# Kernel optimization log

Measured on AMD Instinct MI355X. Metric: run time of the kernel, lower is better.

Reference implementation:

```python
import jax, jax.numpy as jnp
import numpy as np

N_NODES = 50000
N_EDGES = 800000
IN_F = 128
OUT_F = 64
NEG_SLOPE = 0.2  # GATConv default leaky relu slope

def setup_inputs() -> dict:
    key = jax.random.key(0)
    k1, k2, k3, k4, k5 = jax.random.split(key, 5)
    x = jax.random.normal(k1, (N_NODES, IN_F), dtype=jnp.float32)
    edge_index = jax.random.randint(k2, (2, N_EDGES), 0, N_NODES, dtype=jnp.int64)
    W = jax.random.normal(k3, (IN_F, OUT_F), dtype=jnp.float32) * (1.0 / np.sqrt(IN_F))
    att_src = jax.random.normal(k4, (OUT_F,), dtype=jnp.float32) * 0.1
    att_dst = jax.random.normal(k5, (OUT_F,), dtype=jnp.float32) * 0.1
    bias = jnp.zeros((OUT_F,), dtype=jnp.float32)
    return {"x": x, "edge_index": edge_index, "W": W, "att_src": att_src, "att_dst": att_dst, "bias": bias}

def reference(x, edge_index, W, att_src, att_dst, bias):
    N = x.shape[0]
    h = x @ W  # [N, out]
    # GATConv adds self-loops by default
    loops = jnp.arange(N, dtype=edge_index.dtype)
    src = jnp.concatenate([edge_index[0], loops])  # message sources (neighbors j)
    dst = jnp.concatenate([edge_index[1], loops])  # targets i (softmax segments)
    a_src = h @ att_src  # [N]
    a_dst = h @ att_dst  # [N]
    e = a_src[src] + a_dst[dst]  # [E+N]
    e = jnp.where(e > 0, e, NEG_SLOPE * e)
    # segment softmax over incoming edges of each target node
    e_max = jax.ops.segment_max(e, dst, num_segments=N)
    p = jnp.exp(e - e_max[dst])
    denom = jax.ops.segment_sum(p, dst, num_segments=N)
    alpha = p / (denom[dst] + 1e-16)  # [E+N]
    # scatter-add aggregate weighted source features
    out = jax.ops.segment_sum(h[src] * alpha[:, None], dst, num_segments=N)  # [N, out]
    out = jax.nn.relu(out + bias)
    return out[None]  # wrapper unsqueezes: [1, N, out]
```

## Files before the change

### kernel.cpp

```cpp
#include <hip/hip_runtime.h>
#include <math.h>

#define N_NODES 50000
#define N_EDGES 800000
#define IN_F 128
#define OUT_F 64
#define NEG_SLOPE 0.2f

#define CAP 64
#define GB 196
#define TPW 4
#define PSZ 128
#define NPART ((N_NODES + PSZ - 1) / PSZ)
#define PADCAP 3072
#define CHUNK 2048
#define NCHUNK ((N_EDGES + CHUNK - 1) / CHUNK)

typedef __attribute__((ext_vector_type(8))) short bf16x8;
typedef __attribute__((ext_vector_type(4))) float f32x4;

__device__ __forceinline__ unsigned short f2bf(float f) {
    unsigned u = __float_as_uint(f);
    return (unsigned short)((u + 0x7FFFu + ((u >> 16) & 1u)) >> 16);
}
__device__ __forceinline__ float bf_lo(unsigned u) { return __uint_as_float(u << 16); }
__device__ __forceinline__ float bf_hi(unsigned u) { return __uint_as_float(u & 0xFFFF0000u); }

__global__ __launch_bounds__(256) void k_fused(
    const float* __restrict__ x, const float* __restrict__ W,
    const float* __restrict__ att_src, const float* __restrict__ att_dst,
    const int* __restrict__ ei, unsigned short* __restrict__ h,
    float* __restrict__ a_src, float* __restrict__ a_dst,
    int* __restrict__ gcnt, unsigned* __restrict__ glist) {
    int tid = threadIdx.x;

    if (blockIdx.x >= GB) {
        __shared__ int bcnt[NPART];
        __shared__ int bbase[NPART];
        int f = blockIdx.x - GB;
        for (int i = tid; i < NPART; i += 256) bcnt[i] = 0;
        __syncthreads();

        int e0 = f * CHUNK + tid * 8;
        bool val = e0 < N_EDGES;
        int sv[8], dv[8], sl[8];
        if (val) {
            const int4 sa = *reinterpret_cast<const int4*>(ei + e0);
            const int4 sb = *reinterpret_cast<const int4*>(ei + e0 + 4);
            const int4 da = *reinterpret_cast<const int4*>(ei + N_EDGES + e0);
            const int4 db = *reinterpret_cast<const int4*>(ei + N_EDGES + e0 + 4);
            sv[0]=sa.x; sv[1]=sa.y; sv[2]=sa.z; sv[3]=sa.w;
            sv[4]=sb.x; sv[5]=sb.y; sv[6]=sb.z; sv[7]=sb.w;
            dv[0]=da.x; dv[1]=da.y; dv[2]=da.z; dv[3]=da.w;
            dv[4]=db.x; dv[5]=db.y; dv[6]=db.z; dv[7]=db.w;
#pragma unroll
            for (int i = 0; i < 8; ++i)
                sl[i] = atomicAdd(&bcnt[dv[i] >> 7], 1);
        }
        __syncthreads();
        for (int i = tid; i < NPART; i += 256)
            bbase[i] = bcnt[i] ? atomicAdd(&gcnt[i], bcnt[i]) : 0;
        __syncthreads();
        if (val) {
#pragma unroll
            for (int i = 0; i < 8; ++i) {
                int p = dv[i] >> 7;
                int idx = bbase[p] + sl[i];
                if (idx < PADCAP)
                    glist[(size_t)p * PADCAP + idx] =
                        (unsigned)(sv[i] & 0xFFFF) | ((unsigned)(dv[i] & (PSZ - 1)) << 16);
            }
        }
        return;
    }

    int w = tid >> 6;
    int lane = tid & 63;
    int col = lane & 15;
    int kg = lane >> 4;
    int gw = blockIdx.x * 4 + w;

    bf16x8 bf[4][4];
#pragma unroll
    for (int ks = 0; ks < 4; ++ks)
#pragma unroll
        for (int nt = 0; nt < 4; ++nt) {
            bf16x8 b;
#pragma unroll
            for (int i = 0; i < 8; ++i)
                b[i] = (short)f2bf(W[(ks * 32 + kg * 8 + i) * OUT_F + col * 4 + nt]);
            bf[ks][nt] = b;
        }
    float asv[4], adv[4];
#pragma unroll
    for (int nt = 0; nt < 4; ++nt) {
        asv[nt] = att_src[col * 4 + nt];
        adv[nt] = att_dst[col * 4 + nt];
    }

    for (int it = 0; it < TPW; ++it) {
        int r0 = (gw * TPW + it) * 16;
        if (r0 >= N_NODES) break;
        int arow = min(r0 + col, N_NODES - 1);
        const float* xp = &x[(size_t)arow * IN_F + kg * 8];

        bf16x8 af[4];
#pragma unroll
        for (int ks = 0; ks < 4; ++ks) {
            float4 xa = *reinterpret_cast<const float4*>(xp + ks * 32);
            float4 xb = *reinterpret_cast<const float4*>(xp + ks * 32 + 4);
            bf16x8 a;
            a[0] = (short)f2bf(xa.x); a[1] = (short)f2bf(xa.y);
            a[2] = (short)f2bf(xa.z); a[3] = (short)f2bf(xa.w);
            a[4] = (short)f2bf(xb.x); a[5] = (short)f2bf(xb.y);
            a[6] = (short)f2bf(xb.z); a[7] = (short)f2bf(xb.w);
            af[ks] = a;
        }

        f32x4 acc[4];
        f32x4 z = {0.f, 0.f, 0.f, 0.f};
#pragma unroll
        for (int nt = 0; nt < 4; ++nt) acc[nt] = z;
#pragma unroll
        for (int ks = 0; ks < 4; ++ks) {
#pragma unroll
            for (int nt = 0; nt < 4; ++nt)
                acc[nt] = __builtin_amdgcn_mfma_f32_16x16x32_bf16(
                    af[ks], bf[ks][nt], acc[nt], 0, 0, 0);
        }

#pragma unroll
        for (int j = 0; j < 4; ++j) {
            int r = r0 + kg * 4 + j;
            float s1 = acc[0][j] * asv[0] + acc[1][j] * asv[1] +
                       acc[2][j] * asv[2] + acc[3][j] * asv[3];
            float s2 = acc[0][j] * adv[0] + acc[1][j] * adv[1] +
                       acc[2][j] * adv[2] + acc[3][j] * adv[3];
            for (int off = 8; off; off >>= 1) {
                s1 += __shfl_xor(s1, off, 64);
                s2 += __shfl_xor(s2, off, 64);
            }
            if (r < N_NODES) {
                if (col == 0) { a_src[r] = s1; a_dst[r] = s2; }
                ushort4 hv;
                hv.x = f2bf(acc[0][j]);
                hv.y = f2bf(acc[1][j]);
                hv.z = f2bf(acc[2][j]);
                hv.w = f2bf(acc[3][j]);
                *reinterpret_cast<ushort4*>(&h[(size_t)r * OUT_F + col * 4]) = hv;
            }
        }
    }
}

__global__ __launch_bounds__(1024) void k_csr_node(
    const int* __restrict__ gcnt, const unsigned* __restrict__ glist,
    const float* __restrict__ a_src, const float* __restrict__ a_dst,
    const unsigned short* __restrict__ h, const float* __restrict__ bias,
    float* __restrict__ out) {
    __shared__ unsigned short lcsr[PSZ][CAP];
    __shared__ int lcnt[PSZ];
    int p = blockIdx.x;
    int tid = threadIdx.x;
    int n0 = p * PSZ;

    for (int i = tid; i < PSZ; i += 1024) {
        lcnt[i] = 1;
        lcsr[i][0] = (unsigned short)(n0 + i);
    }
    __syncthreads();

    int m = min(gcnt[p], PADCAP);
    size_t base = (size_t)p * PADCAP;
    for (int i = tid; i < m; i += 1024) {
        unsigned u = glist[base + i];
        int dl = u >> 16;
        int k = atomicAdd(&lcnt[dl], 1);
        if (k < CAP) lcsr[dl][k] = (unsigned short)(u & 0xFFFFu);
    }
    __syncthreads();

    int w = tid >> 6;
    int lane = tid & 63;
    int half = lane >> 5;
    int hl = lane & 31;
    int es = hl >> 3;
    int cb = hl & 7;
    int hbase = half << 5;
    int nn_nodes = min(PSZ, N_NODES - n0);

    for (int it = 0; it < PSZ / 32; ++it) {
        int nl = it * 32 + w * 2 + half;
        if (nl >= nn_nodes) continue;
        int node = n0 + nl;
        int n = min(lcnt[nl], CAP);
        float a_d = a_dst[node];
        float acc8[8];
#pragma unroll
        for (int i = 0; i < 8; ++i) acc8[i] = 0.f;
        float l = 0.f;

        if (n <= 32) {
            int s = 0;
            float pp = 0.f;
            if (hl < n) {
                s = lcsr[nl][hl];
                float t = a_src[s] + a_d;
                t = (t > 0.f) ? t : NEG_SLOPE * t;
                pp = __expf(t);
            }
            l = pp;
            for (int off = 16; off; off >>= 1) l += __shfl_xor(l, off, 64);

            int jn = (n + 3) >> 2;
            for (int j = 0; j < jn; ++j) {
                int sl = j * 4 + es;
                float pj = __shfl(pp, hbase + sl, 64);
                int sj = __shfl(s, hbase + sl, 64);
                if (sl < n) {
                    uint4 hv =
                        *reinterpret_cast<const uint4*>(&h[(size_t)sj * OUT_F + cb * 8]);
                    acc8[0] = fmaf(pj, bf_lo(hv.x), acc8[0]);
                    acc8[1] = fmaf(pj, bf_hi(hv.x), acc8[1]);
                    acc8[2] = fmaf(pj, bf_lo(hv.y), acc8[2]);
                    acc8[3] = fmaf(pj, bf_hi(hv.y), acc8[3]);
                    acc8[4] = fmaf(pj, bf_lo(hv.z), acc8[4]);
                    acc8[5] = fmaf(pj, bf_hi(hv.z), acc8[5]);
                    acc8[6] = fmaf(pj, bf_lo(hv.w), acc8[6]);
                    acc8[7] = fmaf(pj, bf_hi(hv.w), acc8[7]);
                }
            }
        } else {
            for (int b2 = 0; b2 < n; b2 += 32) {
                int nn = min(32, n - b2);
                int s = 0;
                float pp = 0.f;
                if (hl < nn) {
                    s = lcsr[nl][b2 + hl];
                    float t = a_src[s] + a_d;
                    t = (t > 0.f) ? t : NEG_SLOPE * t;
                    pp = __expf(t);
                }
                float ps = pp;
                for (int off = 16; off; off >>= 1) ps += __shfl_xor(ps, off, 64);
                l += ps;

                int jn = (nn + 3) >> 2;
                for (int j = 0; j < jn; ++j) {
                    int sl = j * 4 + es;
                    float pj = __shfl(pp, hbase + sl, 64);
                    int sj = __shfl(s, hbase + sl, 64);
                    if (sl < nn) {
                        uint4 hv = *reinterpret_cast<const uint4*>(
                            &h[(size_t)sj * OUT_F + cb * 8]);
                        acc8[0] = fmaf(pj, bf_lo(hv.x), acc8[0]);
                        acc8[1] = fmaf(pj, bf_hi(hv.x), acc8[1]);
                        acc8[2] = fmaf(pj, bf_lo(hv.y), acc8[2]);
                        acc8[3] = fmaf(pj, bf_hi(hv.y), acc8[3]);
                        acc8[4] = fmaf(pj, bf_lo(hv.z), acc8[4]);
                        acc8[5] = fmaf(pj, bf_hi(hv.z), acc8[5]);
                        acc8[6] = fmaf(pj, bf_lo(hv.w), acc8[6]);
                        acc8[7] = fmaf(pj, bf_hi(hv.w), acc8[7]);
                    }
                }
            }
        }

#pragma unroll
        for (int i = 0; i < 8; ++i) {
            acc8[i] += __shfl_xor(acc8[i], 8, 64);
            acc8[i] += __shfl_xor(acc8[i], 16, 64);
        }

        if (hl < 8) {
            float inv = 1.f / (l + 1e-16f);
            const float4 b0 = *reinterpret_cast<const float4*>(&bias[cb * 8]);
            const float4 b1 = *reinterpret_cast<const float4*>(&bias[cb * 8 + 4]);
            float4 o0, o1;
            o0.x = fmaxf(acc8[0] * inv + b0.x, 0.f);
            o0.y = fmaxf(acc8[1] * inv + b0.y, 0.f);
            o0.z = fmaxf(acc8[2] * inv + b0.z, 0.f);
            o0.w = fmaxf(acc8[3] * inv + b0.w, 0.f);
            o1.x = fmaxf(acc8[4] * inv + b1.x, 0.f);
            o1.y = fmaxf(acc8[5] * inv + b1.y, 0.f);
            o1.z = fmaxf(acc8[6] * inv + b1.z, 0.f);
            o1.w = fmaxf(acc8[7] * inv + b1.w, 0.f);
            float* op = &out[(size_t)node * OUT_F + cb * 8];
            *reinterpret_cast<float4*>(op) = o0;
            *reinterpret_cast<float4*>(op + 4) = o1;
        }
    }
}

extern "C" void kernel_launch(void* const* d_in, const int* in_sizes, int n_in,
                              void* d_out, int out_size, void* d_ws, size_t ws_size,
                              hipStream_t stream) {
    const float* x       = (const float*)d_in[0];
    const int*   ei      = (const int*)d_in[1];
    const float* W       = (const float*)d_in[2];
    const float* att_src = (const float*)d_in[3];
    const float* att_dst = (const float*)d_in[4];
    const float* bias    = (const float*)d_in[5];
    float* out = (float*)d_out;

    char* wsp = (char*)d_ws;
    unsigned short* h = (unsigned short*)wsp;
    wsp += (size_t)N_NODES * OUT_F * sizeof(unsigned short);
    float* a_src = (float*)wsp; wsp += (size_t)N_NODES * sizeof(float);
    float* a_dst = (float*)wsp; wsp += (size_t)N_NODES * sizeof(float);
    int*   gcnt  = (int*)wsp;   wsp += (size_t)NPART * sizeof(int);
    wsp = (char*)(((size_t)wsp + 15) & ~(size_t)15);
    unsigned* glist = (unsigned*)wsp;
    wsp += (size_t)NPART * PADCAP * sizeof(unsigned);

    hipMemsetAsync(gcnt, 0, (size_t)NPART * sizeof(int), stream);
    hipLaunchKernelGGL(k_fused, dim3(GB + NCHUNK), dim3(256), 0, stream,
                       x, W, att_src, att_dst, ei, h, a_src, a_dst, gcnt, glist);
    hipLaunchKernelGGL(k_csr_node, dim3(NPART), dim3(1024), 0, stream,
                       gcnt, glist, a_src, a_dst, h, bias, out);
}
```

Baseline: 54.12 us.

## Fold attention vectors into W and compute a_src/a_dst with an extra MFMA

Adds a single-block prep kernel that precomputes W·att_src and W·att_dst as bf16 vectors and zeroes the partition counters, which replaces the memset. In the fused GEMM, one extra 16x16x32 MFMA per k-step produces a_src and a_dst directly. This removes the per-row dot products and cross-lane shuffle reductions. It also drops the row bounds clamps, which holds because N is a multiple of 16, and switches to the library bf16 conversion. In exchange, the attention scores now come from bf16-rounded folded weights, and the launch sequence gains a tiny serial kernel.

```diff
diff --git a/kernel.cpp b/kernel.cpp
--- a/kernel.cpp
+++ b/kernel.cpp
@@ -1,4 +1,5 @@
 #include <hip/hip_runtime.h>
+#include <hip/hip_bf16.h>
 #include <math.h>
 
 #define N_NODES 50000
@@ -19,16 +20,37 @@
 typedef __attribute__((ext_vector_type(8))) short bf16x8;
 typedef __attribute__((ext_vector_type(4))) float f32x4;
 
-__device__ __forceinline__ unsigned short f2bf(float f) {
-    unsigned u = __float_as_uint(f);
-    return (unsigned short)((u + 0x7FFFu + ((u >> 16) & 1u)) >> 16);
+__device__ __forceinline__ short f2bf_s(float f) {
+    return (short)__builtin_bit_cast(unsigned short, __float2bfloat16(f));
+}
+__device__ __forceinline__ unsigned short f2bf_u(float f) {
+    return __builtin_bit_cast(unsigned short, __float2bfloat16(f));
 }
 __device__ __forceinline__ float bf_lo(unsigned u) { return __uint_as_float(u << 16); }
 __device__ __forceinline__ float bf_hi(unsigned u) { return __uint_as_float(u & 0xFFFF0000u); }
 
+__global__ __launch_bounds__(256) void k_prep(
+    const float* __restrict__ W, const float* __restrict__ att_src,
+    const float* __restrict__ att_dst, unsigned short* __restrict__ wa,
+    unsigned short* __restrict__ wd, int* __restrict__ gcnt) {
+    int t = threadIdx.x;
+    for (int i = t; i < NPART; i += 256) gcnt[i] = 0;
+    if (t < IN_F) {
+        float s1 = 0.f, s2 = 0.f;
+        const float* wr = &W[t * OUT_F];
+        for (int c = 0; c < OUT_F; ++c) {
+            float wv = wr[c];
+            s1 = fmaf(wv, att_src[c], s1);
+            s2 = fmaf(wv, att_dst[c], s2);
+        }
+        wa[t] = f2bf_u(s1);
+        wd[t] = f2bf_u(s2);
+    }
+}
+
 __global__ __launch_bounds__(256) void k_fused(
     const float* __restrict__ x, const float* __restrict__ W,
-    const float* __restrict__ att_src, const float* __restrict__ att_dst,
+    const unsigned short* __restrict__ wa, const unsigned short* __restrict__ wd,
     const int* __restrict__ ei, unsigned short* __restrict__ h,
     float* __restrict__ a_src, float* __restrict__ a_dst,
     int* __restrict__ gcnt, unsigned* __restrict__ glist) {
@@ -88,21 +110,22 @@
             bf16x8 b;
 #pragma unroll
             for (int i = 0; i < 8; ++i)
-                b[i] = (short)f2bf(W[(ks * 32 + kg * 8 + i) * OUT_F + col * 4 + nt]);
+                b[i] = f2bf_s(W[(ks * 32 + kg * 8 + i) * OUT_F + col * 4 + nt]);
             bf[ks][nt] = b;
         }
-    float asv[4], adv[4];
-#pragma unroll
-    for (int nt = 0; nt < 4; ++nt) {
-        asv[nt] = att_src[col * 4 + nt];
-        adv[nt] = att_dst[col * 4 + nt];
+    bf16x8 bf5[4];
+#pragma unroll
+    for (int ks = 0; ks < 4; ++ks) {
+        bf16x8 b = {0, 0, 0, 0, 0, 0, 0, 0};
+        if (col == 0) b = *reinterpret_cast<const bf16x8*>(&wa[ks * 32 + kg * 8]);
+        if (col == 1) b = *reinterpret_cast<const bf16x8*>(&wd[ks * 32 + kg * 8]);
+        bf5[ks] = b;
     }
 
     for (int it = 0; it < TPW; ++it) {
         int r0 = (gw * TPW + it) * 16;
         if (r0 >= N_NODES) break;
-        int arow = min(r0 + col, N_NODES - 1);
-        const float* xp = &x[(size_t)arow * IN_F + kg * 8];
+        const float* xp = &x[(size_t)(r0 + col) * IN_F + kg * 8];
 
         bf16x8 af[4];
 #pragma unroll
@@ -110,45 +133,42 @@
             float4 xa = *reinterpret_cast<const float4*>(xp + ks * 32);
             float4 xb = *reinterpret_cast<const float4*>(xp + ks * 32 + 4);
             bf16x8 a;
-            a[0] = (short)f2bf(xa.x); a[1] = (short)f2bf(xa.y);
-            a[2] = (short)f2bf(xa.z); a[3] = (short)f2bf(xa.w);
-            a[4] = (short)f2bf(xb.x); a[5] = (short)f2bf(xb.y);
-            a[6] = (short)f2bf(xb.z); a[7] = (short)f2bf(xb.w);
+            a[0] = f2bf_s(xa.x); a[1] = f2bf_s(xa.y);
+            a[2] = f2bf_s(xa.z); a[3] = f2bf_s(xa.w);
+            a[4] = f2bf_s(xb.x); a[5] = f2bf_s(xb.y);
+            a[6] = f2bf_s(xb.z); a[7] = f2bf_s(xb.w);
             af[ks] = a;
         }
 
-        f32x4 acc[4];
+        f32x4 acc[4], acc5;
         f32x4 z = {0.f, 0.f, 0.f, 0.f};
 #pragma unroll
         for (int nt = 0; nt < 4; ++nt) acc[nt] = z;
+        acc5 = z;
 #pragma unroll
         for (int ks = 0; ks < 4; ++ks) {
 #pragma unroll
             for (int nt = 0; nt < 4; ++nt)
                 acc[nt] = __builtin_amdgcn_mfma_f32_16x16x32_bf16(
                     af[ks], bf[ks][nt], acc[nt], 0, 0, 0);
+            acc5 = __builtin_amdgcn_mfma_f32_16x16x32_bf16(
+                af[ks], bf5[ks], acc5, 0, 0, 0);
         }
 
 #pragma unroll
         for (int j = 0; j < 4; ++j) {
             int r = r0 + kg * 4 + j;
-            float s1 = acc[0][j] * asv[0] + acc[1][j] * asv[1] +
-                       acc[2][j] * asv[2] + acc[3][j] * asv[3];
-            float s2 = acc[0][j] * adv[0] + acc[1][j] * adv[1] +
-                       acc[2][j] * adv[2] + acc[3][j] * adv[3];
-            for (int off = 8; off; off >>= 1) {
-                s1 += __shfl_xor(s1, off, 64);
-                s2 += __shfl_xor(s2, off, 64);
-            }
-            if (r < N_NODES) {
-                if (col == 0) { a_src[r] = s1; a_dst[r] = s2; }
-                ushort4 hv;
-                hv.x = f2bf(acc[0][j]);
-                hv.y = f2bf(acc[1][j]);
-                hv.z = f2bf(acc[2][j]);
-                hv.w = f2bf(acc[3][j]);
-                *reinterpret_cast<ushort4*>(&h[(size_t)r * OUT_F + col * 4]) = hv;
-            }
+            ushort4 hv;
+            hv.x = f2bf_u(acc[0][j]);
+            hv.y = f2bf_u(acc[1][j]);
+            hv.z = f2bf_u(acc[2][j]);
+            hv.w = f2bf_u(acc[3][j]);
+            *reinterpret_cast<ushort4*>(&h[(size_t)r * OUT_F + col * 4]) = hv;
+        }
+        if (col < 2) {
+            float* ap = (col == 0) ? a_src : a_dst;
+#pragma unroll
+            for (int j = 0; j < 4; ++j) ap[r0 + kg * 4 + j] = acc5[j];
         }
     }
 }
@@ -310,12 +330,16 @@
     float* a_dst = (float*)wsp; wsp += (size_t)N_NODES * sizeof(float);
     int*   gcnt  = (int*)wsp;   wsp += (size_t)NPART * sizeof(int);
     wsp = (char*)(((size_t)wsp + 15) & ~(size_t)15);
+    unsigned short* wa = (unsigned short*)wsp; wsp += IN_F * sizeof(unsigned short);
+    unsigned short* wd = (unsigned short*)wsp; wsp += IN_F * sizeof(unsigned short);
+    wsp = (char*)(((size_t)wsp + 15) & ~(size_t)15);
     unsigned* glist = (unsigned*)wsp;
     wsp += (size_t)NPART * PADCAP * sizeof(unsigned);
 
-    hipMemsetAsync(gcnt, 0, (size_t)NPART * sizeof(int), stream);
+    hipLaunchKernelGGL(k_prep, dim3(1), dim3(256), 0, stream,
+                       W, att_src, att_dst, wa, wd, gcnt);
     hipLaunchKernelGGL(k_fused, dim3(GB + NCHUNK), dim3(256), 0, stream,
-                       x, W, att_src, att_dst, ei, h, a_src, a_dst, gcnt, glist);
+                       x, W, wa, wd, ei, h, a_src, a_dst, gcnt, glist);
     hipLaunchKernelGGL(k_csr_node, dim3(NPART), dim3(1024), 0, stream,
                        gcnt, glist, a_src, a_dst, h, bias, out);
 }
```

Measured after the change: 48.85 us. 9.7% less time.
